# Performance work log

Hardware: AMD Instinct MI355X
Metric: run time of the kernel (lower is better)

Reference implementation:

```python
import jax, jax.numpy as jnp
import numpy as np
import itertools

EPS = 1e-3  # BatchNorm1d eps in the original module
N_VOX = 100000


def _build_sparse_structure():
    """Build realistic clustered voxel coords, a 3x3x3 submanifold neighbor
    table (spconv rulebook equivalent), and the unique-merge mapping used by
    sum_duplicates. All index structure is constant (non-differentiable)."""
    rng = np.random.default_rng(0)
    B, Z, Y, X = 2, 40, 1600, 1408  # sparse_shape = grid_size[::-1] + [1,0,0]
    offs01 = np.array(list(itertools.product([0, 1], repeat=3)), dtype=np.int64)
    coords = []
    for b in range(B):
        base = np.stack([rng.integers(0, Z - 1, 13000),
                         rng.integers(0, Y - 1, 13000),
                         rng.integers(0, X - 1, 13000)], 1)
        exp = (base[:, None, :] + offs01[None]).reshape(-1, 3)  # clustered voxels
        coords.append(np.concatenate([np.full((len(exp), 1), b, np.int64), exp], 1))
    coords = np.unique(np.concatenate(coords, 0), axis=0)[:N_VOX]
    assert len(coords) == N_VOX
    # lexicographic unique order => encoded keys are sorted ascending
    key = ((coords[:, 0] * Z + coords[:, 1]) * Y + coords[:, 2]) * X + coords[:, 3]
    offs27 = np.array(list(itertools.product([-1, 0, 1], repeat=3)), np.int64)
    nc = coords[:, None, 1:] + offs27[None]  # [N,27,3]
    inb = (nc >= 0).all(-1) & (nc[..., 0] < Z) & (nc[..., 1] < Y) & (nc[..., 2] < X)
    nk = ((coords[:, None, 0] * Z + nc[..., 0]) * Y + nc[..., 1]) * X + nc[..., 2]
    pos = np.searchsorted(key, nk).clip(0, N_VOX - 1)
    valid = inb & (key[pos] == nk)
    nbr_idx = np.where(valid, pos, -1).astype(np.int32)  # [N,27], -1 = empty
    # second sparse tensor: half its voxels coincide, half are shifted in x
    coords2 = coords.copy()
    coords2[::2, 3] = np.minimum(coords2[::2, 3] + 1, X - 1)
    comb = np.concatenate([coords, coords2], 0)
    uniq, inv = np.unique(comb, axis=0, return_inverse=True)
    return nbr_idx, inv.astype(np.int32), int(len(uniq))


def setup_inputs() -> dict:
    nbr_idx, seg_ids, num_segments = _build_sparse_structure()
    key = jax.random.key(0)
    ks = jax.random.split(key, 6)
    C = 16
    return {
        'voxel_features': jax.random.normal(ks[0], (N_VOX, C), jnp.float32),
        'feat2': jax.random.normal(ks[1], (N_VOX, C), jnp.float32),
        'W0': jax.random.normal(ks[2], (27, C, 16), jnp.float32) * 0.1,
        'g0': jnp.ones((16,), jnp.float32),
        'b0': jnp.zeros((16,), jnp.float32),
        'W1': jax.random.normal(ks[3], (27, 16, 16), jnp.float32) * 0.1,
        'g1': jnp.ones((16,), jnp.float32),
        'b1': jnp.zeros((16,), jnp.float32),
        'Wobo': jax.random.normal(ks[4], (16, 16), jnp.float32) * 0.1,
        'bobo': jnp.zeros((16,), jnp.float32),
        'Wf': jax.random.normal(ks[5], (16, 128), jnp.float32) * 0.1,
        'bf': jnp.zeros((128,), jnp.float32),
        'nbr_idx': jnp.asarray(nbr_idx),
        'seg_ids': jnp.asarray(seg_ids),
        'num_segments': num_segments,
    }


def _subm_bn_relu(x, W, g, b, nbr_idx):
    """Submanifold 3x3x3 sparse conv (gather->GEMM) + BatchNorm1d + ReLU."""
    N = x.shape[0]
    xp = jnp.concatenate([x, jnp.zeros((1, x.shape[1]), x.dtype)], 0)  # pad row
    idx = jnp.where(nbr_idx < 0, N, nbr_idx)  # missing neighbor -> zero row
    y = jnp.einsum('nkc,kco->no', xp[idx], W)  # [N,27,Cin] x [27,Cin,Cout]
    mu = y.mean(0)
    var = y.var(0)
    return jax.nn.relu((y - mu) * jax.lax.rsqrt(var + EPS) * g + b)


def reference(voxel_features, feat2, W0, g0, b0, W1, g1, b1, Wobo, bobo, Wf, bf,
              nbr_idx, seg_ids, num_segments):
    # level-0 conv_input + conv1 (subm conv, BN, ReLU)
    h = _subm_bn_relu(voxel_features, W0, g0, b0, nbr_idx)
    h = _subm_bn_relu(h, W1, g1, b1, nbr_idx)
    # obo_* 1x1 sparse conv on the second branch (plain matmul + bias)
    t2 = feat2 @ Wobo + bobo
    # sum_duplicates: merge coincident sparse indices by summing features
    comb = jnp.concatenate([h, t2], 0)  # [2N,16]
    merged = jax.ops.segment_sum(comb, seg_ids, num_segments=num_segments)
    # final 1x1 sparse conv
    return merged @ Wf + bf  # [U,128]
```

## Files before the change

kernel.cpp:

```cpp
#include <hip/hip_runtime.h>

#define BN_EPS 1e-3f
#define STATC  32

using bfrag  = __attribute__((ext_vector_type(8))) short;
using f32x4v = __attribute__((ext_vector_type(4))) float;

__device__ __forceinline__ unsigned short f2bf(float f) {
    union { float f; unsigned u; } v; v.f = f;
    unsigned r = v.u + 0x7FFFu + ((v.u >> 16) & 1u);
    return (unsigned short)(r >> 16);
}

__global__ __launch_bounds__(256)
void prep_kernel(const float* __restrict__ vf,
                 const float* __restrict__ W0, const float* __restrict__ W1,
                 const float* __restrict__ Wf, const int* __restrict__ seg,
                 unsigned short* __restrict__ xb0,
                 unsigned short* __restrict__ Wb0, unsigned short* __restrict__ Wb1,
                 unsigned short* __restrict__ Wfb,
                 float* __restrict__ stats,
                 int* __restrict__ hidx, int* __restrict__ t2s, int N)
{
    int t = blockIdx.x * 256 + threadIdx.x;
    int TA = 2 * (N + 1);
    unsigned short tmp[8];
    if (t < TA) {
        int n = t >> 1, h = t & 1;
        if (n < N) {
            const f32x4v* yr = (const f32x4v*)(vf + (size_t)n * 16 + h * 8);
            f32x4v v0 = __builtin_nontemporal_load(yr);
            f32x4v v1 = __builtin_nontemporal_load(yr + 1);
#pragma unroll
            for (int j = 0; j < 4; ++j) { tmp[j] = f2bf(v0[j]); tmp[4 + j] = f2bf(v1[j]); }
        } else {
#pragma unroll
            for (int j = 0; j < 8; ++j) tmp[j] = 0;
        }
        *(int4*)(xb0 + (size_t)n * 16 + h * 8) = *(int4*)tmp;
        return;
    }
    t -= TA;
    if (t < 2 * 14 * 64) {
        int w = t >= 896;
        int l = t - w * 896;
        int s = l >> 6, lane = l & 63;
        int q = lane >> 4, n = lane & 15;
        int tap = 2 * s + (q >> 1);
        int cb  = (q & 1) * 8;
        const float* W = w ? W1 : W0;
        unsigned short* Wb = w ? Wb1 : Wb0;
#pragma unroll
        for (int j = 0; j < 8; ++j)
            tmp[j] = (tap < 27) ? f2bf(W[((size_t)(tap * 16 + cb + j)) * 16 + n]) : 0;
        *(int4*)(Wb + (size_t)l * 8) = *(int4*)tmp;
        return;
    }
    t -= 2 * 14 * 64;
    if (t < 512) {
        int ct = t >> 6, lane = t & 63;
        int q = lane >> 4, n = lane & 15;
#pragma unroll
        for (int j = 0; j < 8; ++j)
            tmp[j] = (q < 2) ? f2bf(Wf[(size_t)(q * 8 + j) * 128 + ct * 16 + n]) : 0;
        *(int4*)(Wfb + (size_t)t * 8) = *(int4*)tmp;
        return;
    }
    t -= 512;
    if (t < 2 * STATC * 32) { stats[t] = 0.f; return; }
    t -= 2 * STATC * 32;
    if (t < N) { hidx[seg[t]] = t; return; }
    t -= N;
    if (t < N) {
        int s = seg[N + t];
        if (t == 0 || seg[N + t - 1] != s) t2s[s] = t;
    }
}

__global__ __launch_bounds__(256)
void conv_stats_kernel(const unsigned short* __restrict__ xb,
                       const unsigned short* __restrict__ Wb,
                       const int* __restrict__ nbr,
                       float* __restrict__ y,
                       float* __restrict__ statsC,
                       int N)
{
    __shared__ int   sNbr[64 * 27];
    __shared__ float sred[32];
    int tid = threadIdx.x;
    if (tid < 32) sred[tid] = 0.f;

    int gb = blockIdx.x * 1728;
    int NT = N * 27;
#pragma unroll
    for (int i = 0; i < 7; ++i) {
        int t = i * 256 + tid;
        if (t < 1728) {
            int g = gb + t;
            sNbr[t] = (g < NT) ? __builtin_nontemporal_load(nbr + g) : -1;
        }
    }
    __syncthreads();

    int lane = tid & 63, wib = tid >> 6;
    int q = lane >> 4, m = lane & 15;
    int c0   = (q & 1) * 8;
    int tpar = q >> 1;
    int lvox = wib * 16 + m;
    int base = blockIdx.x * 64 + wib * 16;

    int idx[14];
#pragma unroll
    for (int s = 0; s < 14; ++s) {
        int tap = 2 * s + tpar;
        int id  = (tap < 27) ? sNbr[lvox * 27 + tap] : -1;
        idx[s]  = (id >= 0) ? id : N;
    }

    f32x4v acc = {0.f, 0.f, 0.f, 0.f};
#pragma unroll
    for (int s = 0; s < 14; ++s) {
        bfrag a = *(const bfrag*)(xb + (size_t)idx[s] * 16 + c0);
        bfrag b = *(const bfrag*)(Wb + ((size_t)s * 64 + lane) * 8);
        acc = __builtin_amdgcn_mfma_f32_16x16x32_bf16(a, b, acc, 0, 0, 0);
    }

    int o = lane & 15;
#pragma unroll
    for (int i = 0; i < 4; ++i) {
        int row = base + q * 4 + i;
        if (row < N) y[(size_t)row * 16 + o] = acc[i];
    }
    float s  = acc[0] + acc[1] + acc[2] + acc[3];
    float qq = acc[0] * acc[0] + acc[1] * acc[1] + acc[2] * acc[2] + acc[3] * acc[3];
    s  += __shfl_xor(s, 16);  s  += __shfl_xor(s, 32);
    qq += __shfl_xor(qq, 16); qq += __shfl_xor(qq, 32);
    if (lane < 16) {
        atomicAdd(&sred[lane], s);
        atomicAdd(&sred[16 + lane], qq);
    }
    __syncthreads();
    if (tid < 32)
        atomicAdd(&statsC[(blockIdx.x & (STATC - 1)) * 32 + tid], sred[tid]);
}

__global__ __launch_bounds__(256)
void bnrelu_cvt_kernel(const float* __restrict__ y0, const float* __restrict__ statsC,
                       const float* __restrict__ g, const float* __restrict__ b,
                       float invN, unsigned short* __restrict__ xb, int N)
{
    __shared__ float sred[32];
    __shared__ float sSc[16], sSh[16];
    int tid = threadIdx.x;
    if (tid < 32) {
        float v = 0.f;
#pragma unroll
        for (int k = 0; k < STATC; ++k) v += statsC[k * 32 + tid];
        sred[tid] = v;
    }
    __syncthreads();
    if (tid < 16) {
        float mu  = sred[tid] * invN;
        float var = sred[16 + tid] * invN - mu * mu;
        float sc  = g[tid] * rsqrtf(var + BN_EPS);
        sSc[tid] = sc;
        sSh[tid] = b[tid] - mu * sc;
    }
    __syncthreads();

    int t = blockIdx.x * 256 + tid;
    if (t >= (N + 1) * 2) return;
    int n = t >> 1, h = t & 1;
    unsigned short tmp[8];
    if (n < N) {
        const f32x4v* yr4 = (const f32x4v*)(y0 + (size_t)n * 16 + h * 8);
        f32x4v v0 = __builtin_nontemporal_load(yr4);
        f32x4v v1 = __builtin_nontemporal_load(yr4 + 1);
#pragma unroll
        for (int j = 0; j < 4; ++j) {
            int c = h * 8 + j;
            tmp[j]     = f2bf(fmaxf(fmaf(v0[j], sSc[c], sSh[c]), 0.f));
            tmp[4 + j] = f2bf(fmaxf(fmaf(v1[j], sSc[c + 4], sSh[c + 4]), 0.f));
        }
    } else {
#pragma unroll
        for (int j = 0; j < 8; ++j) tmp[j] = 0;
    }
    *(int4*)(xb + (size_t)n * 16 + h * 8) = *(int4*)tmp;
}

__global__ __launch_bounds__(256)
void merge_final_kernel(const float* __restrict__ y1, const float* __restrict__ statsC,
                        const float* __restrict__ g, const float* __restrict__ b,
                        float invN,
                        const float* __restrict__ feat2, const float* __restrict__ Wobo,
                        const float* __restrict__ bobo,
                        const int* __restrict__ seg,
                        const int* __restrict__ hidx, const int* __restrict__ t2s,
                        const unsigned short* __restrict__ Wfb,
                        const float* __restrict__ bf,
                        float* __restrict__ out, int N, int U)
{
    __shared__ unsigned short smA[64 * 16];
    __shared__ float sred[32];
    __shared__ float sSc[16], sSh[16];
    int tid = threadIdx.x;
    int u0  = blockIdx.x * 64;

    if (tid < 32) {
        float v = 0.f;
#pragma unroll
        for (int k = 0; k < STATC; ++k) v += statsC[k * 32 + tid];
        sred[tid] = v;
    }
    __syncthreads();
    if (tid < 16) {
        float mu  = sred[tid] * invN;
        float var = sred[16 + tid] * invN - mu * mu;
        float sc  = g[tid] * rsqrtf(var + BN_EPS);
        sSc[tid] = sc;
        sSh[tid] = b[tid] - mu * sc;
    }
    __syncthreads();

    if (tid < 128) {
        int sl = tid >> 1, half = tid & 1;
        int u  = u0 + sl;
        float m[8];
#pragma unroll
        for (int j = 0; j < 8; ++j) m[j] = 0.f;
        if (u < U) {
            int hi = hidx[u];
            if ((unsigned)hi < (unsigned)N && seg[hi] == u) {
                const float4* yr = (const float4*)(y1 + (size_t)hi * 16 + half * 8);
                float4 v0 = yr[0], v1 = yr[1];
                float mv[8];
                *(float4*)(mv + 0) = v0; *(float4*)(mv + 4) = v1;
#pragma unroll
                for (int j = 0; j < 8; ++j) {
                    int c = half * 8 + j;
                    m[j] = fmaxf(fmaf(mv[j], sSc[c], sSh[c]), 0.f);
                }
            }
            int r = t2s[u];
            if ((unsigned)r < (unsigned)N && seg[N + r] == u) {
                float a2[8];
#pragma unroll
                for (int j = 0; j < 8; ++j) a2[j] = bobo[half * 8 + j];
                do {
                    const f32x4v* fr = (const f32x4v*)(feat2 + (size_t)r * 16);
                    f32x4v f0 = __builtin_nontemporal_load(fr);
                    f32x4v f1 = __builtin_nontemporal_load(fr + 1);
                    f32x4v f2 = __builtin_nontemporal_load(fr + 2);
                    f32x4v f3 = __builtin_nontemporal_load(fr + 3);
                    float fv[16];
                    *(f32x4v*)(fv + 0)  = f0; *(f32x4v*)(fv + 4)  = f1;
                    *(f32x4v*)(fv + 8)  = f2; *(f32x4v*)(fv + 12) = f3;
#pragma unroll
                    for (int c = 0; c < 16; ++c) {
                        float xc = fv[c];
                        const float* wr = Wobo + c * 16 + half * 8;
#pragma unroll
                        for (int j = 0; j < 8; ++j) a2[j] = fmaf(xc, wr[j], a2[j]);
                    }
                    ++r;
                } while (r < N && seg[N + r] == u);
#pragma unroll
                for (int j = 0; j < 8; ++j) m[j] += a2[j];
            }
        }
        unsigned short tb[8];
#pragma unroll
        for (int j = 0; j < 8; ++j) tb[j] = f2bf(m[j]);
        *(int4*)(smA + (size_t)tid * 8) = *(int4*)tb;
    }
    __syncthreads();

    int lane = tid & 63, w = tid >> 6;
    int q = lane >> 4, n = lane & 15;
    bfrag a = {0, 0, 0, 0, 0, 0, 0, 0};
    if (q < 2)
        a = *(const bfrag*)(smA + ((size_t)(w * 16 + n) * 16 + q * 8));

#pragma unroll
    for (int ct = 0; ct < 8; ++ct) {
        bfrag bb = *(const bfrag*)(Wfb + ((size_t)(ct * 64 + lane)) * 8);
        f32x4v acc = {0.f, 0.f, 0.f, 0.f};
        acc = __builtin_amdgcn_mfma_f32_16x16x32_bf16(a, bb, acc, 0, 0, 0);
        int col = ct * 16 + n;
        float bv = bf[col];
#pragma unroll
        for (int i = 0; i < 4; ++i) {
            int u = u0 + w * 16 + q * 4 + i;
            if (u < U)
                __builtin_nontemporal_store(acc[i] + bv, &out[(size_t)u * 128 + col]);
        }
    }
}

extern "C" void kernel_launch(void* const* d_in, const int* in_sizes, int n_in,
                              void* d_out, int out_size, void* d_ws, size_t ws_size,
                              hipStream_t stream)
{
    const float* vf    = (const float*)d_in[0];
    const float* feat2 = (const float*)d_in[1];
    const float* W0    = (const float*)d_in[2];
    const float* g0    = (const float*)d_in[3];
    const float* b0    = (const float*)d_in[4];
    const float* W1    = (const float*)d_in[5];
    const float* g1    = (const float*)d_in[6];
    const float* b1    = (const float*)d_in[7];
    const float* Wobo  = (const float*)d_in[8];
    const float* bobo  = (const float*)d_in[9];
    const float* Wf    = (const float*)d_in[10];
    const float* bf    = (const float*)d_in[11];
    const int*   nbr   = (const int*)d_in[12];
    const int*   seg   = (const int*)d_in[13];

    int N = in_sizes[0] / 16;
    int U = out_size / 128;

    float* out = (float*)d_out;
    float* ws  = (float*)d_ws;

    int gbConv = (N + 63) / 64;

    float* y0     = ws;
    float* y1     = y0 + (size_t)N * 16;
    float* statsA = y1 + (size_t)N * 16;
    float* statsB = statsA + STATC * 32;
    unsigned short* xb0 = (unsigned short*)(statsB + STATC * 32);
    unsigned short* xb1 = xb0 + (size_t)(N + 1) * 16;
    unsigned short* Wb0 = xb1 + (size_t)(N + 1) * 16;
    unsigned short* Wb1 = Wb0 + 14 * 64 * 8;
    unsigned short* Wfb = Wb1 + 14 * 64 * 8;
    int* hidx = (int*)(Wfb + 8 * 64 * 8);
    int* t2s  = hidx + U;

    float invN  = 1.f / (float)N;
    int thrPrep = 2 * (N + 1) + 2 * 14 * 64 + 512 + 2 * STATC * 32 + 2 * N;
    int gbPrep  = (thrPrep + 255) / 256;
    int gbCvt   = ((N + 1) * 2 + 255) / 256;

    prep_kernel<<<gbPrep, 256, 0, stream>>>(vf, W0, W1, Wf, seg, xb0, Wb0, Wb1,
                                            Wfb, statsA, hidx, t2s, N);
    conv_stats_kernel<<<gbConv, 256, 0, stream>>>(xb0, Wb0, nbr, y0, statsA, N);
    bnrelu_cvt_kernel<<<gbCvt, 256, 0, stream>>>(y0, statsA, g0, b0, invN, xb1, N);
    conv_stats_kernel<<<gbConv, 256, 0, stream>>>(xb1, Wb1, nbr, y1, statsB, N);
    merge_final_kernel<<<(U + 63) / 64, 256, 0, stream>>>(y1, statsB, g1, b1, invN,
                                                          feat2, Wobo, bobo, seg,
                                                          hidx, t2s, Wfb, bf, out, N, U);
}
```

Before: 177.1 us.

## Stage conv output through LDS and widen merge kernel to 128 rows

```diff
diff --git a/kernel.cpp b/kernel.cpp
--- a/kernel.cpp
+++ b/kernel.cpp
@@ -2,6 +2,7 @@
 
 #define BN_EPS 1e-3f
 #define STATC  32
+#define MBLK   128
 
 using bfrag  = __attribute__((ext_vector_type(8))) short;
 using f32x4v = __attribute__((ext_vector_type(4))) float;
@@ -86,6 +87,7 @@
                        int N)
 {
     __shared__ int   sNbr[64 * 27];
+    __shared__ float sY[64 * 16];
     __shared__ float sred[32];
     int tid = threadIdx.x;
     if (tid < 32) sred[tid] = 0.f;
@@ -107,7 +109,6 @@
     int c0   = (q & 1) * 8;
     int tpar = q >> 1;
     int lvox = wib * 16 + m;
-    int base = blockIdx.x * 64 + wib * 16;
 
     int idx[14];
 #pragma unroll
@@ -127,10 +128,9 @@
 
     int o = lane & 15;
 #pragma unroll
-    for (int i = 0; i < 4; ++i) {
-        int row = base + q * 4 + i;
-        if (row < N) y[(size_t)row * 16 + o] = acc[i];
-    }
+    for (int i = 0; i < 4; ++i)
+        sY[(wib * 16 + q * 4 + i) * 16 + o] = acc[i];
+
     float s  = acc[0] + acc[1] + acc[2] + acc[3];
     float qq = acc[0] * acc[0] + acc[1] * acc[1] + acc[2] * acc[2] + acc[3] * acc[3];
     s  += __shfl_xor(s, 16);  s  += __shfl_xor(s, 32);
@@ -140,6 +140,13 @@
         atomicAdd(&sred[16 + lane], qq);
     }
     __syncthreads();
+
+    {
+        int row = blockIdx.x * 64 + (tid >> 2);
+        if (row < N)
+            *(f32x4v*)(y + (size_t)row * 16 + (tid & 3) * 4) =
+                *(const f32x4v*)(sY + (size_t)(tid >> 2) * 16 + (tid & 3) * 4);
+    }
     if (tid < 32)
         atomicAdd(&statsC[(blockIdx.x & (STATC - 1)) * 32 + tid], sred[tid]);
 }
@@ -201,11 +208,11 @@
                         const float* __restrict__ bf,
                         float* __restrict__ out, int N, int U)
 {
-    __shared__ unsigned short smA[64 * 16];
+    __shared__ unsigned short smA[MBLK * 16];
     __shared__ float sred[32];
     __shared__ float sSc[16], sSh[16];
     int tid = threadIdx.x;
-    int u0  = blockIdx.x * 64;
+    int u0  = blockIdx.x * MBLK;
 
     if (tid < 32) {
         float v = 0.f;
@@ -223,51 +230,63 @@
     }
     __syncthreads();
 
-    if (tid < 128) {
+    {
         int sl = tid >> 1, half = tid & 1;
         int u  = u0 + sl;
+        bool valid = u < U;
+        int uc = valid ? u : 0;
+        int hi = hidx[uc];
+        int r  = t2s[uc];
+        bool hasH = valid && (unsigned)hi < (unsigned)N && seg[hi] == u;
+        bool hasT = valid && (unsigned)r  < (unsigned)N && seg[N + r] == u;
+
+        size_t hoff = (size_t)(hasH ? hi : 0) * 16 + half * 8;
+        f32x4v yv0 = *(const f32x4v*)(y1 + hoff);
+        f32x4v yv1 = *(const f32x4v*)(y1 + hoff + 4);
+        size_t toff = (size_t)(hasT ? r : 0) * 16;
+        f32x4v f0 = __builtin_nontemporal_load((const f32x4v*)(feat2 + toff));
+        f32x4v f1 = __builtin_nontemporal_load((const f32x4v*)(feat2 + toff) + 1);
+        f32x4v f2 = __builtin_nontemporal_load((const f32x4v*)(feat2 + toff) + 2);
+        f32x4v f3 = __builtin_nontemporal_load((const f32x4v*)(feat2 + toff) + 3);
+
         float m[8];
 #pragma unroll
         for (int j = 0; j < 8; ++j) m[j] = 0.f;
-        if (u < U) {
-            int hi = hidx[u];
-            if ((unsigned)hi < (unsigned)N && seg[hi] == u) {
-                const float4* yr = (const float4*)(y1 + (size_t)hi * 16 + half * 8);
-                float4 v0 = yr[0], v1 = yr[1];
-                float mv[8];
-                *(float4*)(mv + 0) = v0; *(float4*)(mv + 4) = v1;
-#pragma unroll
-                for (int j = 0; j < 8; ++j) {
-                    int c = half * 8 + j;
-                    m[j] = fmaxf(fmaf(mv[j], sSc[c], sSh[c]), 0.f);
+        if (hasH) {
+#pragma unroll
+            for (int j = 0; j < 4; ++j) {
+                int c = half * 8 + j;
+                m[j]     = fmaxf(fmaf(yv0[j], sSc[c],     sSh[c]),     0.f);
+                m[4 + j] = fmaxf(fmaf(yv1[j], sSc[c + 4], sSh[c + 4]), 0.f);
+            }
+        }
+        if (hasT) {
+            float a2[8];
+#pragma unroll
+            for (int j = 0; j < 8; ++j) a2[j] = bobo[half * 8 + j];
+            float fv[16];
+            *(f32x4v*)(fv + 0)  = f0; *(f32x4v*)(fv + 4)  = f1;
+            *(f32x4v*)(fv + 8)  = f2; *(f32x4v*)(fv + 12) = f3;
+            for (;;) {
+#pragma unroll
+                for (int c = 0; c < 16; ++c) {
+                    float xc = fv[c];
+                    const float* wr = Wobo + c * 16 + half * 8;
+#pragma unroll
+                    for (int j = 0; j < 8; ++j) a2[j] = fmaf(xc, wr[j], a2[j]);
                 }
+                ++r;
+                if (r >= N || seg[N + r] != u) break;
+                const f32x4v* fr = (const f32x4v*)(feat2 + (size_t)r * 16);
+                f32x4v g0 = __builtin_nontemporal_load(fr);
+                f32x4v g1 = __builtin_nontemporal_load(fr + 1);
+                f32x4v g2 = __builtin_nontemporal_load(fr + 2);
+                f32x4v g3 = __builtin_nontemporal_load(fr + 3);
+                *(f32x4v*)(fv + 0)  = g0; *(f32x4v*)(fv + 4)  = g1;
+                *(f32x4v*)(fv + 8)  = g2; *(f32x4v*)(fv + 12) = g3;
             }
-            int r = t2s[u];
-            if ((unsigned)r < (unsigned)N && seg[N + r] == u) {
-                float a2[8];
-#pragma unroll
-                for (int j = 0; j < 8; ++j) a2[j] = bobo[half * 8 + j];
-                do {
-                    const f32x4v* fr = (const f32x4v*)(feat2 + (size_t)r * 16);
-                    f32x4v f0 = __builtin_nontemporal_load(fr);
-                    f32x4v f1 = __builtin_nontemporal_load(fr + 1);
-                    f32x4v f2 = __builtin_nontemporal_load(fr + 2);
-                    f32x4v f3 = __builtin_nontemporal_load(fr + 3);
-                    float fv[16];
-                    *(f32x4v*)(fv + 0)  = f0; *(f32x4v*)(fv + 4)  = f1;
-                    *(f32x4v*)(fv + 8)  = f2; *(f32x4v*)(fv + 12) = f3;
-#pragma unroll
-                    for (int c = 0; c < 16; ++c) {
-                        float xc = fv[c];
-                        const float* wr = Wobo + c * 16 + half * 8;
-#pragma unroll
-                        for (int j = 0; j < 8; ++j) a2[j] = fmaf(xc, wr[j], a2[j]);
-                    }
-                    ++r;
-                } while (r < N && seg[N + r] == u);
-#pragma unroll
-                for (int j = 0; j < 8; ++j) m[j] += a2[j];
-            }
+#pragma unroll
+            for (int j = 0; j < 8; ++j) m[j] += a2[j];
         }
         unsigned short tb[8];
 #pragma unroll
@@ -278,22 +297,24 @@
 
     int lane = tid & 63, w = tid >> 6;
     int q = lane >> 4, n = lane & 15;
-    bfrag a = {0, 0, 0, 0, 0, 0, 0, 0};
-    if (q < 2)
-        a = *(const bfrag*)(smA + ((size_t)(w * 16 + n) * 16 + q * 8));
-
-#pragma unroll
-    for (int ct = 0; ct < 8; ++ct) {
-        bfrag bb = *(const bfrag*)(Wfb + ((size_t)(ct * 64 + lane)) * 8);
-        f32x4v acc = {0.f, 0.f, 0.f, 0.f};
-        acc = __builtin_amdgcn_mfma_f32_16x16x32_bf16(a, bb, acc, 0, 0, 0);
-        int col = ct * 16 + n;
-        float bv = bf[col];
-#pragma unroll
-        for (int i = 0; i < 4; ++i) {
-            int u = u0 + w * 16 + q * 4 + i;
-            if (u < U)
-                __builtin_nontemporal_store(acc[i] + bv, &out[(size_t)u * 128 + col]);
+#pragma unroll
+    for (int rt = 0; rt < 2; ++rt) {
+        int row0 = w * 32 + rt * 16;
+        bfrag a = {0, 0, 0, 0, 0, 0, 0, 0};
+        if (q < 2)
+            a = *(const bfrag*)(smA + ((size_t)(row0 + n) * 16 + q * 8));
+#pragma unroll
+        for (int ct = 0; ct < 8; ++ct) {
+            bfrag bb = *(const bfrag*)(Wfb + ((size_t)(ct * 64 + lane)) * 8);
+            f32x4v acc = {0.f, 0.f, 0.f, 0.f};
+            acc = __builtin_amdgcn_mfma_f32_16x16x32_bf16(a, bb, acc, 0, 0, 0);
+            int col = ct * 16 + n;
+            float bv = bf[col];
+#pragma unroll
+            for (int i = 0; i < 4; ++i) {
+                int u = u0 + row0 + q * 4 + i;
+                if (u < U) out[(size_t)u * 128 + col] = acc[i] + bv;
+            }
         }
     }
 }
@@ -341,13 +362,14 @@
     int thrPrep = 2 * (N + 1) + 2 * 14 * 64 + 512 + 2 * STATC * 32 + 2 * N;
     int gbPrep  = (thrPrep + 255) / 256;
     int gbCvt   = ((N + 1) * 2 + 255) / 256;
+    int gbMerge = (U + MBLK - 1) / MBLK;
 
     prep_kernel<<<gbPrep, 256, 0, stream>>>(vf, W0, W1, Wf, seg, xb0, Wb0, Wb1,
                                             Wfb, statsA, hidx, t2s, N);
     conv_stats_kernel<<<gbConv, 256, 0, stream>>>(xb0, Wb0, nbr, y0, statsA, N);
     bnrelu_cvt_kernel<<<gbCvt, 256, 0, stream>>>(y0, statsA, g0, b0, invN, xb1, N);
     conv_stats_kernel<<<gbConv, 256, 0, stream>>>(xb1, Wb1, nbr, y1, statsB, N);
-    merge_final_kernel<<<(U + 63) / 64, 256, 0, stream>>>(y1, statsB, g1, b1, invN,
-                                                          feat2, Wobo, bobo, seg,
-                                                          hidx, t2s, Wfb, bf, out, N, U);
-}
+    merge_final_kernel<<<gbMerge, 256, 0, stream>>>(y1, statsB, g1, b1, invN,
+                                                    feat2, Wobo, bobo, seg,
+                                                    hidx, t2s, Wfb, bf, out, N, U);
+}
```

After: 165.0 us. 1.07x faster.
